# Performance work log

Hardware: AMD Instinct MI355X
Metric: run time of the kernel (lower is better)

The kernel has to match this reference:

```python
import jax, jax.numpy as jnp
import numpy as np

N = 10000      # num nodes
E = 320000     # num edges
IN = 256       # in_dim
MP = 256       # mp_width
FL = 512       # fl_width
OUT = 64       # out_dim


def setup_inputs() -> dict:
    key = jax.random.key(0)
    ks = jax.random.split(key, 20)
    inp = {}
    inp["x"] = jax.random.normal(ks[0], (N, IN), dtype=jnp.float32)
    inp["edge_index"] = jax.random.randint(ks[1], (2, E), 0, N, dtype=jnp.int64)
    # iMP (frozen) linear layers: weight ~ N(0, 1) per nn.init.normal_(std=1.0)
    inp["mp_w0"] = jax.random.normal(ks[2], (IN, MP), dtype=jnp.float32)
    inp["mp_b0"] = jax.random.uniform(ks[3], (MP,), minval=-1.0, maxval=1.0) / np.sqrt(IN)
    inp["mp_w1"] = jax.random.normal(ks[4], (MP, MP), dtype=jnp.float32)
    inp["mp_b1"] = jax.random.uniform(ks[5], (MP,), minval=-1.0, maxval=1.0) / np.sqrt(MP)
    inp["mp_w2"] = jax.random.normal(ks[6], (MP, MP), dtype=jnp.float32)
    inp["mp_b2"] = jax.random.uniform(ks[7], (MP,), minval=-1.0, maxval=1.0) / np.sqrt(MP)
    # FC layers (torch default Linear init scale ~ 1/sqrt(fan_in))
    inp["fc_w0"] = jax.random.normal(ks[8], (MP, FL), dtype=jnp.float32) / np.sqrt(MP)
    inp["fc_b0"] = jnp.zeros((FL,), dtype=jnp.float32)
    inp["fc_w1"] = jax.random.normal(ks[9], (FL, FL), dtype=jnp.float32) / np.sqrt(FL)
    inp["fc_b1"] = jnp.zeros((FL,), dtype=jnp.float32)
    # injection projections
    inp["inj_w0"] = jax.random.normal(ks[10], (MP, FL), dtype=jnp.float32) / np.sqrt(MP)
    inp["inj_b0"] = jnp.zeros((FL,), dtype=jnp.float32)
    inp["inj_w1"] = jax.random.normal(ks[11], (MP, FL), dtype=jnp.float32) / np.sqrt(MP)
    inp["inj_b1"] = jnp.zeros((FL,), dtype=jnp.float32)
    inp["alpha"] = jnp.array(1.0, dtype=jnp.float32)
    inp["out_w"] = jax.random.normal(ks[12], (FL, OUT), dtype=jnp.float32) / np.sqrt(FL)
    inp["out_b"] = jnp.zeros((OUT,), dtype=jnp.float32)
    return inp


def _imp(x, w, b, row, col, deg_inv):
    # h = relu(W x); h /= deg; Ah = scatter_add over row of h[col]
    h = jax.nn.relu(x @ w + b) * deg_inv[:, None]      # [N, out]
    return jnp.zeros_like(h).at[row].add(h[col])       # gather + scatter-add


def reference(x, edge_index, mp_w0, mp_b0, mp_w1, mp_b1, mp_w2, mp_b2,
              fc_w0, fc_b0, fc_w1, fc_b1, inj_w0, inj_b0, inj_w1, inj_b1,
              alpha, out_w, out_b):
    row, col = edge_index[0], edge_index[1]
    deg = jax.ops.segment_sum(jnp.ones((E,), x.dtype), col, num_segments=N)
    # nodes with deg==0 never appear in col so clamping does not change output
    deg_inv = 1.0 / jnp.maximum(deg, 1.0)

    h = _imp(x, mp_w0, mp_b0, row, col, deg_inv)
    h = _imp(h, mp_w1, mp_b1, row, col, deg_inv)
    h = _imp(h, mp_w2, mp_b2, row, col, deg_inv)

    x_inject = h
    h = alpha * (jax.nn.relu(h) @ fc_w0 + fc_b0) + (x_inject @ inj_w0 + inj_b0)
    h = alpha * (jax.nn.relu(h) @ fc_w1 + fc_b1) + (x_inject @ inj_w1 + inj_b1)
    return h @ out_w + out_b
```

## Files before the change

### kernel.cpp

```cpp
#include <hip/hip_runtime.h>

#define N_NODES 10000
#define N_EDGES 320000
#define MPAD 10112
#define NBIN 10048
#define CHUNK 2048
#define NCH 157
#define CAP 128
#define PREP_BLOCKS 512
#define PREP_TOT 1148480L

typedef unsigned short u16;
typedef short bf16x8 __attribute__((ext_vector_type(8)));
typedef float f32x4 __attribute__((ext_vector_type(4)));

__device__ __forceinline__ u16 f2b(float f) {
  unsigned u = __builtin_bit_cast(unsigned, f);
  unsigned r = u + 0x7fffu + ((u >> 16) & 1u);
  return (u16)(r >> 16);
}
__device__ __forceinline__ unsigned pack2(float a, float b) {
  return (unsigned)f2b(a) | ((unsigned)f2b(b) << 16);
}
__device__ __forceinline__ float blo(unsigned u) { return __builtin_bit_cast(float, u << 16); }
__device__ __forceinline__ float bhi(unsigned u) { return __builtin_bit_cast(float, u & 0xffff0000u); }

struct PP {
  const float *x; const int *ei;
  const float *w0, *w1, *w2, *fcw0, *injw0, *fcw1, *injw1, *outw;
  const float *fcb0, *injb0, *fcb1, *injb1, *alpha, *outb;
  u16 *xb, *w0t, *w1t, *w2t, *wc1t, *wft;
  float *bias1, *bf;
  unsigned *histRC;
};

__global__ __launch_bounds__(256) void prep_hist(PP P) {
  __shared__ unsigned sh[NBIN];
  const int tid = threadIdx.x, bid = blockIdx.x;
  const float alpha = P.alpha[0];

  if (bid < NCH) {
    for (int i = tid; i < NBIN; i += 256) sh[i] = 0;
    __syncthreads();
    const int e0 = bid * CHUNK;
    for (int j = tid; j < CHUNK; j += 256) {
      int e = e0 + j;
      if (e < N_EDGES) {
        atomicAdd(&sh[P.ei[e]], 1u);
        atomicAdd(&sh[P.ei[N_EDGES + e]], 65536u);
      }
    }
    __syncthreads();
    for (int i = tid; i < NBIN; i += 256)
      P.histRC[(size_t)bid * NBIN + i] = sh[i];
    return;
  }

  const long stride = (long)PREP_BLOCKS * 256;
  for (long ii = (long)(bid - NCH) * 256 + tid; ii < PREP_TOT; ii += stride) {
    long i = ii;
    if (i < 640000L) {
      float4 v = ((const float4*)P.x)[i];
      uint2 o;
      o.x = pack2(v.x, v.y);
      o.y = pack2(v.z, v.w);
      *(uint2*)(P.xb + 4 * i) = o;
      continue;
    }
    i -= 640000L;
    if (i < 65536) { P.w0t[i] = f2b(P.w0[(i & 255) * 256 + (i >> 8)]); continue; }
    i -= 65536;
    if (i < 65536) { P.w1t[i] = f2b(P.w1[(i & 255) * 256 + (i >> 8)]); continue; }
    i -= 65536;
    if (i < 65536) { P.w2t[i] = f2b(P.w2[(i & 255) * 256 + (i >> 8)]); continue; }
    i -= 65536;
    if (i < 262144) {
      int n = (int)(i >> 9), k = (int)(i & 511);
      float v = (k < 256) ? alpha * P.fcw0[k * 512 + n] : P.injw0[(k - 256) * 512 + n];
      P.wc1t[i] = f2b(v); continue;
    }
    i -= 262144;
    if (i < 49152) {
      int n = (int)(i & 63), k = (int)(i >> 6);
      float acc = 0.f;
      if (k < 512) {
        const float* fr = P.fcw1 + (size_t)k * 512;
#pragma unroll 8
        for (int j = 0; j < 512; ++j) acc += fr[j] * P.outw[j * 64 + n];
        acc *= alpha;
      } else {
        const float* ir = P.injw1 + (size_t)(k - 512) * 512;
#pragma unroll 8
        for (int j = 0; j < 512; ++j) acc += ir[j] * P.outw[j * 64 + n];
      }
      P.wft[n * 768 + k] = f2b(acc);
      continue;
    }
    i -= 49152;
    if (i < 64) {
      float acc = P.outb[i];
#pragma unroll 8
      for (int j = 0; j < 512; ++j)
        acc += (alpha * P.fcb1[j] + P.injb1[j]) * P.outw[j * 64 + i];
      P.bf[i] = acc;
      continue;
    }
    i -= 64;
    if (i < 512) { P.bias1[i] = alpha * P.fcb0[i] + P.injb0[i]; continue; }
  }
}

__global__ __launch_bounds__(64) void col_scan(const unsigned* __restrict__ histRC,
                                               u16* __restrict__ chunkoff,
                                               int* __restrict__ cnt,
                                               float* __restrict__ deg_inv) {
  int r = blockIdx.x * 64 + threadIdx.x;
  if (r >= MPAD) return;
  if (r >= NBIN) { deg_inv[r] = 1.0f; return; }
  unsigned run = 0;
#pragma unroll 8
  for (int ch = 0; ch < NCH; ++ch) {
    chunkoff[(size_t)ch * NBIN + r] = (u16)(run & 0xffffu);
    run += histRC[(size_t)ch * NBIN + r];
  }
  int cr = (int)(run & 0xffffu);
  int dg = (int)(run >> 16);
  cnt[r] = cr;
  deg_inv[r] = 1.0f / (float)(dg > 1 ? dg : 1);
}

__global__ __launch_bounds__(256) void place_edges(const int* __restrict__ ei,
                                                   const u16* __restrict__ chunkoff,
                                                   int* __restrict__ csr) {
  __shared__ int cur[NBIN];
  const int ch = blockIdx.x, t = threadIdx.x;
  const u16* co = chunkoff + (size_t)ch * NBIN;
  for (int i = t; i < NBIN; i += 256) cur[i] = co[i];
  __syncthreads();
  const int e0 = ch * CHUNK;
#pragma unroll
  for (int j = 0; j < CHUNK; j += 256) {
    int e = e0 + j + t;
    if (e < N_EDGES) {
      int r = ei[e];
      int c = ei[N_EDGES + e];
      int rank = atomicAdd(&cur[r], 1);
      if (rank < CAP) csr[r * CAP + rank] = c;
    }
  }
}

template<int K, bool RELU, bool SCALE, bool F32OUT>
__global__ __launch_bounds__(128) void gemm64(
    const u16* __restrict__ A, int lda,
    const u16* __restrict__ Bt,
    const float* __restrict__ bias,
    const float* __restrict__ scale,
    u16* __restrict__ Cb, float* __restrict__ Cf, int ldc)
{
  __shared__ u16 As[64 * 72];
  __shared__ u16 Bs[64 * 72];
  const int tid = threadIdx.x;
  const int m0 = blockIdx.x * 64;
  const int n0 = blockIdx.y * 64;
  const int wave = tid >> 6;
  const int lane = tid & 63;
  const int wr = wave * 32;
  const int lm = lane & 15;
  const int koff = (lane >> 4) * 8;

  const int srow = tid >> 2;
  const int scol = (tid & 3) * 16;
  const u16* Ag0 = A + (size_t)(m0 + srow) * lda + scol;
  const u16* Ag1 = A + (size_t)(m0 + srow + 32) * lda + scol;
  const u16* Bg0 = Bt + (size_t)(n0 + srow) * K + scol;
  const u16* Bg1 = Bt + (size_t)(n0 + srow + 32) * K + scol;
  u16* Asw0 = &As[srow * 72 + scol];
  u16* Asw1 = &As[(srow + 32) * 72 + scol];
  u16* Bsw0 = &Bs[srow * 72 + scol];
  u16* Bsw1 = &Bs[(srow + 32) * 72 + scol];

  f32x4 acc[2][4] = {};

  int4 pa0 = *(const int4*)(Ag0),     pa1 = *(const int4*)(Ag0 + 8);
  int4 pa2 = *(const int4*)(Ag1),     pa3 = *(const int4*)(Ag1 + 8);
  int4 pb0 = *(const int4*)(Bg0),     pb1 = *(const int4*)(Bg0 + 8);
  int4 pb2 = *(const int4*)(Bg1),     pb3 = *(const int4*)(Bg1 + 8);

#pragma unroll
  for (int kb = 0; kb < K; kb += 64) {
    __syncthreads();
    *(int4*)Asw0 = pa0; *(int4*)(Asw0 + 8) = pa1;
    *(int4*)Asw1 = pa2; *(int4*)(Asw1 + 8) = pa3;
    *(int4*)Bsw0 = pb0; *(int4*)(Bsw0 + 8) = pb1;
    *(int4*)Bsw1 = pb2; *(int4*)(Bsw1 + 8) = pb3;
    __syncthreads();
    if (kb + 64 < K) {
      pa0 = *(const int4*)(Ag0 + kb + 64); pa1 = *(const int4*)(Ag0 + kb + 72);
      pa2 = *(const int4*)(Ag1 + kb + 64); pa3 = *(const int4*)(Ag1 + kb + 72);
      pb0 = *(const int4*)(Bg0 + kb + 64); pb1 = *(const int4*)(Bg0 + kb + 72);
      pb2 = *(const int4*)(Bg1 + kb + 64); pb3 = *(const int4*)(Bg1 + kb + 72);
    }
#pragma unroll
    for (int ks = 0; ks < 2; ++ks) {
      bf16x8 af[2], bf[4];
#pragma unroll
      for (int mi = 0; mi < 2; ++mi)
        af[mi] = *(const bf16x8*)&As[(wr + mi * 16 + lm) * 72 + ks * 32 + koff];
#pragma unroll
      for (int ni = 0; ni < 4; ++ni)
        bf[ni] = *(const bf16x8*)&Bs[(ni * 16 + lm) * 72 + ks * 32 + koff];
#pragma unroll
      for (int mi = 0; mi < 2; ++mi)
#pragma unroll
        for (int ni = 0; ni < 4; ++ni)
          acc[mi][ni] = __builtin_amdgcn_mfma_f32_16x16x32_bf16(af[mi], bf[ni], acc[mi][ni], 0, 0, 0);
    }
  }

  const int q4 = (lane >> 4) * 4;
#pragma unroll
  for (int mi = 0; mi < 2; ++mi) {
#pragma unroll
    for (int ni = 0; ni < 4; ++ni) {
      const int gc = n0 + ni * 16 + lm;
      const float bv = bias[gc];
#pragma unroll
      for (int r = 0; r < 4; ++r) {
        const int gr = m0 + wr + mi * 16 + q4 + r;
        float v = acc[mi][ni][r] + bv;
        if (RELU) v = fmaxf(v, 0.f);
        if (SCALE) v *= scale[gr];
        if (F32OUT) {
          if (gr < N_NODES) Cf[(size_t)gr * ldc + gc] = v;
        } else {
          Cb[(size_t)gr * ldc + gc] = f2b(v);
        }
      }
    }
  }
}

__global__ __launch_bounds__(256) void aggregate(
    const u16* __restrict__ tmp, const int* __restrict__ cnt,
    const int* __restrict__ csr, u16* __restrict__ out0,
    u16* __restrict__ A1, u16* __restrict__ A2, int mode)
{
  const int wv = threadIdx.x >> 6;
  const int lane = threadIdx.x & 63;
  const int r = blockIdx.x * 4 + wv;
  const int half = lane >> 5;
  const int q = lane & 31;
  const int beg = r * CAP, end = beg + cnt[r];
  const size_t feat = (size_t)q * 16;
  const char* tb = (const char*)tmp;

  float s0 = 0.f, s1 = 0.f, s2 = 0.f, s3 = 0.f, s4 = 0.f, s5 = 0.f, s6 = 0.f, s7 = 0.f;
  int i = beg;
  for (; i + 8 <= end; i += 8) {
    uint4 v[4];
#pragma unroll
    for (int j = 0; j < 4; ++j)
      v[j] = *(const uint4*)(tb + (size_t)csr[i + 2 * j + half] * 512 + feat);
#pragma unroll
    for (int j = 0; j < 4; ++j) {
      s0 += blo(v[j].x); s1 += bhi(v[j].x); s2 += blo(v[j].y); s3 += bhi(v[j].y);
      s4 += blo(v[j].z); s5 += bhi(v[j].z); s6 += blo(v[j].w); s7 += bhi(v[j].w);
    }
  }
  for (; i < end; i += 2) {
    int id = i + half;
    if (id < end) {
      uint4 v = *(const uint4*)(tb + (size_t)csr[id] * 512 + feat);
      s0 += blo(v.x); s1 += bhi(v.x); s2 += blo(v.y); s3 += bhi(v.y);
      s4 += blo(v.z); s5 += bhi(v.z); s6 += blo(v.w); s7 += bhi(v.w);
    }
  }
  const int src = lane ^ 32;
  s0 += __shfl(s0, src, 64); s1 += __shfl(s1, src, 64);
  s2 += __shfl(s2, src, 64); s3 += __shfl(s3, src, 64);
  s4 += __shfl(s4, src, 64); s5 += __shfl(s5, src, 64);
  s6 += __shfl(s6, src, 64); s7 += __shfl(s7, src, 64);

  if (half == 0) {
    uint4 pv;
    pv.x = pack2(s0, s1); pv.y = pack2(s2, s3);
    pv.z = pack2(s4, s5); pv.w = pack2(s6, s7);
    if (mode == 0) {
      *(uint4*)((char*)out0 + (size_t)r * 512 + feat) = pv;
    } else {
      uint4 pr;
      pr.x = pack2(fmaxf(s0, 0.f), fmaxf(s1, 0.f));
      pr.y = pack2(fmaxf(s2, 0.f), fmaxf(s3, 0.f));
      pr.z = pack2(fmaxf(s4, 0.f), fmaxf(s5, 0.f));
      pr.w = pack2(fmaxf(s6, 0.f), fmaxf(s7, 0.f));
      *(uint4*)((char*)A1 + (size_t)r * 1024 + feat) = pr;
      *(uint4*)((char*)A1 + (size_t)r * 1024 + 512 + feat) = pv;
      *(uint4*)((char*)A2 + (size_t)r * 1536 + 1024 + feat) = pv;
    }
  }
}

extern "C" void kernel_launch(void* const* d_in, const int* in_sizes, int n_in,
                              void* d_out, int out_size, void* d_ws, size_t ws_size,
                              hipStream_t stream) {
  const int* ei = (const int*)d_in[1];

  char* p = (char*)d_ws;
  auto carve = [&](size_t bytes) -> void* {
    void* r = (void*)p;
    p += (bytes + 255) & ~(size_t)255;
    return r;
  };
  unsigned* histRC  = (unsigned*)carve((size_t)NCH * NBIN * 4);
  u16*    chunkoff  = (u16*)carve((size_t)NCH * NBIN * 2);
  int*    cnt       = (int*)carve(NBIN * 4);
  int*    csr       = (int*)carve((size_t)NBIN * CAP * 4);
  float*  deg_inv   = (float*)carve(MPAD * 4);
  float*  bias1     = (float*)carve(512 * 4);
  float*  bf        = (float*)carve(64 * 4);
  u16* xb   = (u16*)carve((size_t)MPAD * 256 * 2);
  u16* w0t  = (u16*)carve(65536 * 2);
  u16* w1t  = (u16*)carve(65536 * 2);
  u16* w2t  = (u16*)carve(65536 * 2);
  u16* wc1t = (u16*)carve(262144 * 2);
  u16* wft  = (u16*)carve(49152 * 2);
  u16* tmp  = (u16*)carve((size_t)MPAD * 256 * 2);
  u16* h    = (u16*)carve((size_t)MPAD * 256 * 2);
  u16* cat1 = (u16*)carve((size_t)MPAD * 512 * 2);
  u16* cat2 = (u16*)carve((size_t)MPAD * 768 * 2);

  PP pp;
  pp.x = (const float*)d_in[0];
  pp.ei = ei;
  pp.w0 = (const float*)d_in[2];
  pp.w1 = (const float*)d_in[4];
  pp.w2 = (const float*)d_in[6];
  pp.fcw0 = (const float*)d_in[8];
  pp.fcw1 = (const float*)d_in[10];
  pp.injw0 = (const float*)d_in[12];
  pp.injw1 = (const float*)d_in[14];
  pp.outw = (const float*)d_in[17];
  pp.fcb0 = (const float*)d_in[9];
  pp.injb0 = (const float*)d_in[13];
  pp.fcb1 = (const float*)d_in[11];
  pp.injb1 = (const float*)d_in[15];
  pp.alpha = (const float*)d_in[16];
  pp.outb = (const float*)d_in[18];
  pp.xb = xb; pp.w0t = w0t; pp.w1t = w1t; pp.w2t = w2t;
  pp.wc1t = wc1t; pp.wft = wft;
  pp.bias1 = bias1; pp.bf = bf;
  pp.histRC = histRC;

  const float* mp_b0 = (const float*)d_in[3];
  const float* mp_b1 = (const float*)d_in[5];
  const float* mp_b2 = (const float*)d_in[7];
  float* out = (float*)d_out;

  prep_hist<<<NCH + PREP_BLOCKS, 256, 0, stream>>>(pp);
  col_scan<<<MPAD / 64, 64, 0, stream>>>(histRC, chunkoff, cnt, deg_inv);
  place_edges<<<NCH, 256, 0, stream>>>(ei, chunkoff, csr);

  dim3 gmp(MPAD / 64, 4), gfc(MPAD / 64, 8), go(MPAD / 64, 1);
  gemm64<256, true, true, false><<<gmp, 128, 0, stream>>>(xb, 256, w0t, mp_b0, deg_inv, tmp, nullptr, 256);
  aggregate<<<2500, 256, 0, stream>>>(tmp, cnt, csr, h, nullptr, nullptr, 0);
  gemm64<256, true, true, false><<<gmp, 128, 0, stream>>>(h, 256, w1t, mp_b1, deg_inv, tmp, nullptr, 256);
  aggregate<<<2500, 256, 0, stream>>>(tmp, cnt, csr, h, nullptr, nullptr, 0);
  gemm64<256, true, true, false><<<gmp, 128, 0, stream>>>(h, 256, w2t, mp_b2, deg_inv, tmp, nullptr, 256);
  aggregate<<<2500, 256, 0, stream>>>(tmp, cnt, csr, nullptr, cat1, cat2, 1);
  gemm64<512, true, false, false><<<gfc, 128, 0, stream>>>(cat1, 512, wc1t, bias1, nullptr, cat2, nullptr, 768);
  gemm64<768, false, false, true><<<go, 128, 0, stream>>>(cat2, 768, wft, bf, nullptr, nullptr, out, 64);
}
```

Before: 245.1 us.

## Split edge histogram from weight prep, vectorize weight fold, deepen aggregate unroll

```diff
diff --git a/kernel.cpp b/kernel.cpp
--- a/kernel.cpp
+++ b/kernel.cpp
@@ -26,38 +26,37 @@
 __device__ __forceinline__ float bhi(unsigned u) { return __builtin_bit_cast(float, u & 0xffff0000u); }
 
 struct PP {
-  const float *x; const int *ei;
+  const float *x;
   const float *w0, *w1, *w2, *fcw0, *injw0, *fcw1, *injw1, *outw;
   const float *fcb0, *injb0, *fcb1, *injb1, *alpha, *outb;
   u16 *xb, *w0t, *w1t, *w2t, *wc1t, *wft;
   float *bias1, *bf;
-  unsigned *histRC;
 };
 
-__global__ __launch_bounds__(256) void prep_hist(PP P) {
+__global__ __launch_bounds__(256) void edge_hist(const int* __restrict__ ei,
+                                                 unsigned* __restrict__ histRC) {
   __shared__ unsigned sh[NBIN];
-  const int tid = threadIdx.x, bid = blockIdx.x;
+  const int tid = threadIdx.x, ch = blockIdx.x;
+  for (int i = tid; i < NBIN; i += 256) sh[i] = 0;
+  __syncthreads();
+  const int e0 = ch * CHUNK;
+#pragma unroll
+  for (int j = 0; j < CHUNK; j += 256) {
+    int e = e0 + j + tid;
+    if (e < N_EDGES) {
+      atomicAdd(&sh[ei[e]], 1u);
+      atomicAdd(&sh[ei[N_EDGES + e]], 65536u);
+    }
+  }
+  __syncthreads();
+  for (int i = tid; i < NBIN; i += 256)
+    histRC[(size_t)ch * NBIN + i] = sh[i];
+}
+
+__global__ __launch_bounds__(256) void prep(PP P) {
   const float alpha = P.alpha[0];
-
-  if (bid < NCH) {
-    for (int i = tid; i < NBIN; i += 256) sh[i] = 0;
-    __syncthreads();
-    const int e0 = bid * CHUNK;
-    for (int j = tid; j < CHUNK; j += 256) {
-      int e = e0 + j;
-      if (e < N_EDGES) {
-        atomicAdd(&sh[P.ei[e]], 1u);
-        atomicAdd(&sh[P.ei[N_EDGES + e]], 65536u);
-      }
-    }
-    __syncthreads();
-    for (int i = tid; i < NBIN; i += 256)
-      P.histRC[(size_t)bid * NBIN + i] = sh[i];
-    return;
-  }
-
   const long stride = (long)PREP_BLOCKS * 256;
-  for (long ii = (long)(bid - NCH) * 256 + tid; ii < PREP_TOT; ii += stride) {
+  for (long ii = (long)blockIdx.x * 256 + threadIdx.x; ii < PREP_TOT; ii += stride) {
     long i = ii;
     if (i < 640000L) {
       float4 v = ((const float4*)P.x)[i];
@@ -82,17 +81,19 @@
     i -= 262144;
     if (i < 49152) {
       int n = (int)(i & 63), k = (int)(i >> 6);
-      float acc = 0.f;
-      if (k < 512) {
-        const float* fr = P.fcw1 + (size_t)k * 512;
-#pragma unroll 8
-        for (int j = 0; j < 512; ++j) acc += fr[j] * P.outw[j * 64 + n];
-        acc *= alpha;
-      } else {
-        const float* ir = P.injw1 + (size_t)(k - 512) * 512;
-#pragma unroll 8
-        for (int j = 0; j < 512; ++j) acc += ir[j] * P.outw[j * 64 + n];
+      const float* fr = (k < 512) ? P.fcw1 + (size_t)k * 512
+                                  : P.injw1 + (size_t)(k - 512) * 512;
+      float a0 = 0.f, a1 = 0.f, a2 = 0.f, a3 = 0.f;
+#pragma unroll 4
+      for (int j = 0; j < 512; j += 4) {
+        float4 f = *(const float4*)(fr + j);
+        a0 += f.x * P.outw[(j + 0) * 64 + n];
+        a1 += f.y * P.outw[(j + 1) * 64 + n];
+        a2 += f.z * P.outw[(j + 2) * 64 + n];
+        a3 += f.w * P.outw[(j + 3) * 64 + n];
       }
+      float acc = (a0 + a1) + (a2 + a3);
+      if (k < 512) acc *= alpha;
       P.wft[n * 768 + k] = f2b(acc);
       continue;
     }
@@ -257,6 +258,17 @@
 
   float s0 = 0.f, s1 = 0.f, s2 = 0.f, s3 = 0.f, s4 = 0.f, s5 = 0.f, s6 = 0.f, s7 = 0.f;
   int i = beg;
+  for (; i + 16 <= end; i += 16) {
+    uint4 v[8];
+#pragma unroll
+    for (int j = 0; j < 8; ++j)
+      v[j] = *(const uint4*)(tb + (size_t)csr[i + 2 * j + half] * 512 + feat);
+#pragma unroll
+    for (int j = 0; j < 8; ++j) {
+      s0 += blo(v[j].x); s1 += bhi(v[j].x); s2 += blo(v[j].y); s3 += bhi(v[j].y);
+      s4 += blo(v[j].z); s5 += bhi(v[j].z); s6 += blo(v[j].w); s7 += bhi(v[j].w);
+    }
+  }
   for (; i + 8 <= end; i += 8) {
     uint4 v[4];
 #pragma unroll
@@ -332,7 +344,6 @@
 
   PP pp;
   pp.x = (const float*)d_in[0];
-  pp.ei = ei;
   pp.w0 = (const float*)d_in[2];
   pp.w1 = (const float*)d_in[4];
   pp.w2 = (const float*)d_in[6];
@@ -350,14 +361,14 @@
   pp.xb = xb; pp.w0t = w0t; pp.w1t = w1t; pp.w2t = w2t;
   pp.wc1t = wc1t; pp.wft = wft;
   pp.bias1 = bias1; pp.bf = bf;
-  pp.histRC = histRC;
 
   const float* mp_b0 = (const float*)d_in[3];
   const float* mp_b1 = (const float*)d_in[5];
   const float* mp_b2 = (const float*)d_in[7];
   float* out = (float*)d_out;
 
-  prep_hist<<<NCH + PREP_BLOCKS, 256, 0, stream>>>(pp);
+  edge_hist<<<NCH, 256, 0, stream>>>(ei, histRC);
+  prep<<<PREP_BLOCKS, 256, 0, stream>>>(pp);
   col_scan<<<MPAD / 64, 64, 0, stream>>>(histRC, chunkoff, cnt, deg_inv);
   place_edges<<<NCH, 256, 0, stream>>>(ei, chunkoff, csr);
 
```

Result: slower. 250.5 us (+2.2%).
